# Optimization experiments

Measured on AMD Instinct MI355X. Metric: run time of the kernel, lower is better.

The kernel has to match this reference:

```python
import jax, jax.numpy as jnp
import numpy as np

C = 1024          # channels
RED = 16          # reduction
RC = C // RED     # 64 bottleneck channels
BZ, NUM_PROPS = 4, 256
BP = BZ * NUM_PROPS


def setup_inputs() -> dict:
    key = jax.random.key(0)
    ks = jax.random.split(key, 10)
    x_props = jax.random.normal(ks[0], (BP, C, 7, 7), dtype=jnp.float32)
    x_query = jax.random.normal(ks[1], (BZ, C, 8, 8), dtype=jnp.float32)
    s_conv = 1.0 / np.sqrt(C)   # kaiming-uniform-ish for conv1d 1x1 (fan_in=C)
    s_mlp = 1.0 / np.sqrt(RC)   # Linear fan_in = RC
    pc_w = jax.random.uniform(ks[2], (RC, C), minval=-s_conv, maxval=s_conv)
    pc_b = jax.random.uniform(ks[3], (RC,), minval=-s_conv, maxval=s_conv)
    qc_w = jax.random.uniform(ks[4], (RC, C), minval=-s_conv, maxval=s_conv)
    qc_b = jax.random.uniform(ks[5], (RC,), minval=-s_conv, maxval=s_conv)
    pm_w = jax.random.uniform(ks[6], (C, RC), minval=-s_mlp, maxval=s_mlp)
    pm_b = jax.random.uniform(ks[7], (C,), minval=-s_mlp, maxval=s_mlp)
    qm_w = jax.random.uniform(ks[8], (C, RC), minval=-s_mlp, maxval=s_mlp)
    qm_b = jax.random.uniform(ks[9], (C,), minval=-s_mlp, maxval=s_mlp)
    return {"x_props": x_props, "x_query": x_query,
            "pc_w": pc_w, "pc_b": pc_b, "qc_w": qc_w, "qc_b": qc_b,
            "pm_w": pm_w, "pm_b": pm_b, "qm_w": qm_w, "qm_b": qm_b}


def reference(x_props, x_query, pc_w, pc_b, qc_w, qc_b, pm_w, pm_b, qm_w, qm_b):
    bp, c, hp, wp = x_props.shape
    bz, _, hq, wq = x_query.shape
    n = bp // bz
    L = hp * wp
    # bilinear resize (half-pixel centers == torch align_corners=False)
    r_query = jax.image.resize(x_query, (bz, c, hp, wp), method='bilinear')
    # 1x1 conv bottlenecks (conv1d over flattened spatial dim)
    q_feat = jnp.einsum('rc,bcl->brl', qc_w, r_query.reshape(bz, c, L)) + qc_b[None, :, None]   # [bz, RC, L]
    p_feat = jnp.einsum('rc,bcl->brl', pc_w, x_props.reshape(bp, c, L)) + pc_b[None, :, None]   # [bp, RC, L]
    # similarity contracts spatial dim; query feature shared across props of same image
    p_feat_g = p_feat.reshape(bz, n, -1, L)
    sim = jnp.einsum('bnrl,bsl->bnrs', p_feat_g, q_feat)                                        # [bz, n, RC, RC]
    p_rel = sim.mean(axis=3).reshape(bp, -1)                                                    # [bp, RC]
    q_rel = sim.mean(axis=2).reshape(bp, -1)                                                    # [bp, RC]
    # channel-gate MLPs
    p_att = jax.nn.sigmoid(p_rel @ pm_w.T + pm_b)                                               # [bp, C]
    q_att = jax.nn.sigmoid(q_rel @ qm_w.T + qm_b)                                               # [bp, C]
    # co-excitation
    f_props = x_props * p_att[:, :, None, None]
    xq_rep = jnp.broadcast_to(x_query[:, None], (bz, n, c, hq, wq)).reshape(bp, c, hq, wq)
    f_query = xq_rep * q_att[:, :, None, None]
    return f_props, f_query, p_att.reshape(bp, c, 1, 1)
```

## Files before the change

kernel.cpp:

```cpp
#include <hip/hip_runtime.h>


typedef float v4f __attribute__((ext_vector_type(4)));

#define WQBAR  0
#define WPCBW  320
#define WPCBB  1344
#define WQF    1408
#define WPMBF  14336
#define WQMBF  47104
#define WQATT  79872

#define OUT_FP 0
#define OUT_FQ 51380224
#define OUT_PA 118489088

__device__ __forceinline__ float sigmoidf(float v) {
    return 1.0f / (1.0f + __expf(-v));
}
__device__ __forceinline__ unsigned short bf16_rne(float x) {
    unsigned u = __float_as_uint(x);
    return (unsigned short)((u + 0x7FFFu + ((u >> 16) & 1u)) >> 16);
}
__device__ __forceinline__ unsigned div49(unsigned e) {
    return __umulhi(e, 2804876602u) >> 5;
}

__global__ __launch_bounds__(1024) void k_prepall(
    const float* __restrict__ xq, const float* __restrict__ qc_w,
    const float* __restrict__ qc_b, const float* __restrict__ pc_w,
    const float* __restrict__ pc_b, const float* __restrict__ pm_w,
    const float* __restrict__ qm_w, float* __restrict__ ws)
{
    const int blk = blockIdx.x, t = threadIdx.x;
    if (blk < 196) {
        __shared__ float rq[1024];
        __shared__ float qf_s[64];
        const int b = blk / 49, l = blk - b * 49;
        const int wave = t >> 6, lane = t & 63;
        const int i = l / 7, j = l - i * 7;
        float fi = (2 * i + 1) * (1.0f / 14.0f);
        float fj = (2 * j + 1) * (1.0f / 14.0f);
        float wi0 = (1.0f - 0.875f * fi) * (1.0f / 1.125f); float wi1 = 1.0f - wi0;
        float wj0 = (1.0f - 0.875f * fj) * (1.0f / 1.125f); float wj1 = 1.0f - wj0;
        const float* X = xq + ((size_t)(b * 1024 + t) << 6);
        rq[t] = wi0 * (wj0 * X[i * 8 + j]       + wj1 * X[i * 8 + j + 1])
              + wi1 * (wj0 * X[(i + 1) * 8 + j] + wj1 * X[(i + 1) * 8 + j + 1]);
        __syncthreads();
        #pragma unroll
        for (int ii = 0; ii < 4; ++ii) {
            int s = wave * 4 + ii;
            const float* wr = qc_w + s * 1024;
            float part = 0.0f;
            #pragma unroll
            for (int k = 0; k < 16; ++k) part += wr[k * 64 + lane] * rq[k * 64 + lane];
            #pragma unroll
            for (int off = 32; off; off >>= 1) part += __shfl_down(part, off, 64);
            if (lane == 0) {
                float val = part + qc_b[s];
                ws[WQF + b * 3136 + s * 49 + l] = val;
                qf_s[s] = val;
            }
        }
        __syncthreads();
        if (t == 0) {
            float s = 0.0f;
            #pragma unroll
            for (int k = 0; k < 64; ++k) s += qf_s[k];
            ws[WQBAR + b * 49 + l] = s * (1.0f / 64.0f);
        }
    } else if (blk == 196) {
        float s = 0.0f;
        for (int r = 0; r < 64; ++r) s += pc_w[r * 1024 + t];
        ws[WPCBW + t] = s * (1.0f / 64.0f);
        if (t == 0) {
            float sb = 0.0f;
            for (int r = 0; r < 64; ++r) sb += pc_b[r];
            ws[WPCBB] = sb * (1.0f / 64.0f);
        }
    } else {
        int idx = (blk - 197) * 1024 + t;
        int r = (idx & 65535) >> 10, c = idx & 1023;
        float w = (idx < 65536) ? pm_w[c * 64 + r] : qm_w[c * 64 + r];
        unsigned short* dst = (unsigned short*)(ws + (idx < 65536 ? WPMBF : WQMBF));
        dst[idx & 65535] = bf16_rne(w);
    }
}

__global__ __launch_bounds__(256) void k_red(
    const float* __restrict__ x,
    const float* __restrict__ pc_w, const float* __restrict__ pc_b,
    const float* __restrict__ pm_b, const float* __restrict__ qm_b,
    float* __restrict__ ws, float* __restrict__ patt_out)
{
    __shared__ float xs[6272];
    __shared__ float y_s[1024];
    __shared__ float pcb_s[1024];
    __shared__ float qbar_s[49];
    __shared__ float sq_s;
    __shared__ float pbar_part[2][49];
    __shared__ float pbar_s[49];
    __shared__ float prel_s[64];
    __shared__ float qrel_s[64];

    const int t = threadIdx.x, wave = t >> 6, lane = t & 63;
    const int p = blockIdx.x, b = p >> 8;

    if (t < 49) qbar_s[t] = ws[WQBAR + b * 49 + t];
    for (int k = t; k < 1024; k += 256) pcb_s[k] = ws[WPCBW + k];
    const float pcbarb = ws[WPCBB];

    const float4* xp4 = (const float4*)(x + (size_t)p * 50176);
    float pbar_acc = 0.0f;

    for (int ch = 0; ch < 8; ++ch) {
        __syncthreads();
        const float4* src = xp4 + ch * 1568;
        float4* xs4 = (float4*)xs;
        for (int k = t; k < 1568; k += 256) xs4[k] = src[k];
        __syncthreads();
        if (ch == 0 && t == 0) {
            float s = 0.0f;
            #pragma unroll
            for (int l = 0; l < 49; ++l) s += qbar_s[l];
            sq_s = s;
        }
        if (wave < 2) {
            int c = wave * 64 + lane;
            const float* row = xs + c * 49;
            float acc = 0.0f;
            #pragma unroll
            for (int l = 0; l < 49; ++l) acc += row[l] * qbar_s[l];
            y_s[ch * 128 + c] = acc;
        } else if (lane < 49) {
            int cw = (wave - 2) * 64;
            const float* base = xs + cw * 49 + lane;
            const float* pw = pcb_s + ch * 128 + cw;
            float a = 0.0f;
            #pragma unroll
            for (int c = 0; c < 64; ++c) a += pw[c] * base[c * 49];
            pbar_acc += a;
        }
    }
    if (wave >= 2 && lane < 49) pbar_part[wave - 2][lane] = pbar_acc;
    __syncthreads();
    if (t < 49) pbar_s[t] = pbar_part[0][t] + pbar_part[1][t] + pcbarb;
    __syncthreads();
    const float sumqbar = sq_s;

    #pragma unroll
    for (int i = 0; i < 16; ++i) {
        int r = wave * 16 + i;
        const float* wr = pc_w + r * 1024;
        float part = 0.0f;
        #pragma unroll
        for (int k = 0; k < 16; ++k) part += wr[k * 64 + lane] * y_s[k * 64 + lane];
        #pragma unroll
        for (int off = 32; off; off >>= 1) part += __shfl_down(part, off, 64);
        if (lane == 0) prel_s[r] = part + pc_b[r] * sumqbar;
    }
    if (t < 64) {
        const float* qfr = ws + WQF + (b * 3136 + t * 49);
        float a = 0.0f;
        #pragma unroll
        for (int l = 0; l < 49; ++l) a += pbar_s[l] * qfr[l];
        qrel_s[t] = a;
    }
    __syncthreads();

    {
        const unsigned* wp = (const unsigned*)(ws + WPMBF);
        const unsigned* wq = (const unsigned*)(ws + WQMBF);
        float4 ap = {0, 0, 0, 0}, aq = {0, 0, 0, 0};
        #pragma unroll
        for (int r = 0; r < 64; ++r) {
            float pr = prel_s[r], qr = qrel_s[r];
            unsigned p01 = wp[r * 512 + 2 * t];
            unsigned p23 = wp[r * 512 + 2 * t + 1];
            ap.x += __uint_as_float(p01 << 16) * pr;
            ap.y += __uint_as_float(p01 & 0xFFFF0000u) * pr;
            ap.z += __uint_as_float(p23 << 16) * pr;
            ap.w += __uint_as_float(p23 & 0xFFFF0000u) * pr;
            unsigned q01 = wq[r * 512 + 2 * t];
            unsigned q23 = wq[r * 512 + 2 * t + 1];
            aq.x += __uint_as_float(q01 << 16) * qr;
            aq.y += __uint_as_float(q01 & 0xFFFF0000u) * qr;
            aq.z += __uint_as_float(q23 << 16) * qr;
            aq.w += __uint_as_float(q23 & 0xFFFF0000u) * qr;
        }
        float4 pb = ((const float4*)pm_b)[t];
        float4 qb = ((const float4*)qm_b)[t];
        float4 po, qo;
        po.x = sigmoidf(ap.x + pb.x); po.y = sigmoidf(ap.y + pb.y);
        po.z = sigmoidf(ap.z + pb.z); po.w = sigmoidf(ap.w + pb.w);
        qo.x = sigmoidf(aq.x + qb.x); qo.y = sigmoidf(aq.y + qb.y);
        qo.z = sigmoidf(aq.z + qb.z); qo.w = sigmoidf(aq.w + qb.w);
        ((float4*)patt_out)[p * 256 + t] = po;
        ((float4*)(ws + WQATT))[p * 256 + t] = qo;
    }
}

__global__ __launch_bounds__(256) void k_scale(
    const float* __restrict__ x, const float* __restrict__ xq,
    const float* __restrict__ patt, const float* __restrict__ qatt,
    float* __restrict__ fprops, float* __restrict__ fquery)
{
    const unsigned NP4 = 12845056u;
    const unsigned NT4 = 29622272u;
    const unsigned stride = gridDim.x * blockDim.x;
    for (unsigned i = blockIdx.x * blockDim.x + threadIdx.x; i < NT4; i += stride) {
        if (i < NP4) {
            unsigned e = i * 4u;
            unsigned q = div49(e);
            unsigned m = e - 49u * q;
            float a0 = patt[q];
            float a1 = patt[q + (m >= 46u)];
            v4f v = ((const v4f*)x)[i];
            v4f g;
            g.x = a0;
            g.y = (m >= 48u) ? a1 : a0;
            g.z = (m >= 47u) ? a1 : a0;
            g.w = (m >= 46u) ? a1 : a0;
            __builtin_nontemporal_store(v * g, (v4f*)fprops + i);
        } else {
            unsigned j = i - NP4;
            unsigned p = j >> 14;
            unsigned k = j & 16383u;
            float att = qatt[(p << 10) | (k >> 4)];
            v4f v = ((const v4f*)xq)[(((size_t)(p >> 8)) << 14) | k];
            __builtin_nontemporal_store(v * att, (v4f*)fquery + j);
        }
    }
}

extern "C" void kernel_launch(void* const* d_in, const int* in_sizes, int n_in,
                              void* d_out, int out_size, void* d_ws, size_t ws_size,
                              hipStream_t stream) {
    const float* x_props = (const float*)d_in[0];
    const float* x_query = (const float*)d_in[1];
    const float* pc_w    = (const float*)d_in[2];
    const float* pc_b    = (const float*)d_in[3];
    const float* qc_w    = (const float*)d_in[4];
    const float* qc_b    = (const float*)d_in[5];
    const float* pm_w    = (const float*)d_in[6];
    const float* pm_b    = (const float*)d_in[7];
    const float* qm_w    = (const float*)d_in[8];
    const float* qm_b    = (const float*)d_in[9];
    float* out = (float*)d_out;
    float* ws  = (float*)d_ws;

    k_prepall<<<325, 1024, 0, stream>>>(x_query, qc_w, qc_b, pc_w, pc_b, pm_w, qm_w, ws);
    k_red<<<1024, 256, 0, stream>>>(x_props, pc_w, pc_b, pm_b, qm_b, ws, out + OUT_PA);
    k_scale<<<8192, 256, 0, stream>>>(x_props, x_query, out + OUT_PA, ws + WQATT,
                                      out + OUT_FP, out + OUT_FQ);
}
```

Before: 172.9 us.

## Fuse query scaling into reduction kernel, keep q_att in shared memory

```diff
diff --git a/kernel.cpp b/kernel.cpp
--- a/kernel.cpp
+++ b/kernel.cpp
@@ -9,7 +9,6 @@
 #define WQF    1408
 #define WPMBF  14336
 #define WQMBF  47104
-#define WQATT  79872
 
 #define OUT_FP 0
 #define OUT_FQ 51380224
@@ -88,10 +87,11 @@
 }
 
 __global__ __launch_bounds__(256) void k_red(
-    const float* __restrict__ x,
+    const float* __restrict__ x, const float* __restrict__ xq,
     const float* __restrict__ pc_w, const float* __restrict__ pc_b,
     const float* __restrict__ pm_b, const float* __restrict__ qm_b,
-    float* __restrict__ ws, float* __restrict__ patt_out)
+    float* __restrict__ ws, float* __restrict__ patt_out,
+    float* __restrict__ fquery)
 {
     __shared__ float xs[6272];
     __shared__ float y_s[1024];
@@ -196,40 +196,40 @@
         qo.x = sigmoidf(aq.x + qb.x); qo.y = sigmoidf(aq.y + qb.y);
         qo.z = sigmoidf(aq.z + qb.z); qo.w = sigmoidf(aq.w + qb.w);
         ((float4*)patt_out)[p * 256 + t] = po;
-        ((float4*)(ws + WQATT))[p * 256 + t] = qo;
+        ((float4*)pcb_s)[t] = qo;
+    }
+    __syncthreads();
+
+    const v4f* xq4 = (const v4f*)(xq + ((size_t)b << 16));
+    v4f* fq4 = (v4f*)(fquery + ((size_t)p << 16));
+    #pragma unroll
+    for (int i = 0; i < 64; ++i) {
+        int k = i * 256 + t;
+        float att = pcb_s[k >> 4];
+        v4f v = xq4[k];
+        __builtin_nontemporal_store(v * att, fq4 + k);
     }
 }
 
 __global__ __launch_bounds__(256) void k_scale(
-    const float* __restrict__ x, const float* __restrict__ xq,
-    const float* __restrict__ patt, const float* __restrict__ qatt,
-    float* __restrict__ fprops, float* __restrict__ fquery)
+    const float* __restrict__ x, const float* __restrict__ patt,
+    float* __restrict__ fprops)
 {
-    const unsigned NP4 = 12845056u;
-    const unsigned NT4 = 29622272u;
+    const unsigned N4 = 12845056u;
     const unsigned stride = gridDim.x * blockDim.x;
-    for (unsigned i = blockIdx.x * blockDim.x + threadIdx.x; i < NT4; i += stride) {
-        if (i < NP4) {
-            unsigned e = i * 4u;
-            unsigned q = div49(e);
-            unsigned m = e - 49u * q;
-            float a0 = patt[q];
-            float a1 = patt[q + (m >= 46u)];
-            v4f v = ((const v4f*)x)[i];
-            v4f g;
-            g.x = a0;
-            g.y = (m >= 48u) ? a1 : a0;
-            g.z = (m >= 47u) ? a1 : a0;
-            g.w = (m >= 46u) ? a1 : a0;
-            __builtin_nontemporal_store(v * g, (v4f*)fprops + i);
-        } else {
-            unsigned j = i - NP4;
-            unsigned p = j >> 14;
-            unsigned k = j & 16383u;
-            float att = qatt[(p << 10) | (k >> 4)];
-            v4f v = ((const v4f*)xq)[(((size_t)(p >> 8)) << 14) | k];
-            __builtin_nontemporal_store(v * att, (v4f*)fquery + j);
-        }
+    for (unsigned i = blockIdx.x * blockDim.x + threadIdx.x; i < N4; i += stride) {
+        unsigned e = i * 4u;
+        unsigned q = div49(e);
+        unsigned m = e - 49u * q;
+        float a0 = patt[q];
+        float a1 = patt[q + (m >= 46u)];
+        v4f v = ((const v4f*)x)[i];
+        v4f g;
+        g.x = a0;
+        g.y = (m >= 48u) ? a1 : a0;
+        g.z = (m >= 47u) ? a1 : a0;
+        g.w = (m >= 46u) ? a1 : a0;
+        __builtin_nontemporal_store(v * g, (v4f*)fprops + i);
     }
 }
 
@@ -250,7 +250,7 @@
     float* ws  = (float*)d_ws;
 
     k_prepall<<<325, 1024, 0, stream>>>(x_query, qc_w, qc_b, pc_w, pc_b, pm_w, qm_w, ws);
-    k_red<<<1024, 256, 0, stream>>>(x_props, pc_w, pc_b, pm_b, qm_b, ws, out + OUT_PA);
-    k_scale<<<8192, 256, 0, stream>>>(x_props, x_query, out + OUT_PA, ws + WQATT,
-                                      out + OUT_FP, out + OUT_FQ);
-}
+    k_red<<<1024, 256, 0, stream>>>(x_props, x_query, pc_w, pc_b, pm_b, qm_b, ws,
+                                    out + OUT_PA, out + OUT_FQ);
+    k_scale<<<4096, 256, 0, stream>>>(x_props, out + OUT_PA, out + OUT_FP);
+}
```

Measured after the change: 168.0 us. 1.03x faster.
